# Optimization experiments

Hardware: AMD Instinct MI355X
Metric: run time of the kernel (lower is better)

Reference implementation:

```python
import jax, jax.numpy as jnp
import numpy as np

HIDDEN = 896
N_HEADS = 14
N_KV = 2
HEAD_DIM = HIDDEN // N_HEADS  # 64
N_REP = N_HEADS // N_KV       # 7
ROPE_THETA = 1000000.0


def setup_inputs() -> dict:
    key = jax.random.key(0)
    ks = jax.random.split(key, 8)
    B, S = 2, 2048
    s = 0.02
    return {
        "hidden_states": jax.random.normal(ks[0], (B, S, HIDDEN), dtype=jnp.float32),
        "position_ids": jnp.broadcast_to(jnp.arange(S, dtype=jnp.int64), (B, S)),
        "Wq": jax.random.normal(ks[1], (HIDDEN, HIDDEN), dtype=jnp.float32) * s,
        "bq": jnp.zeros((HIDDEN,), dtype=jnp.float32),
        "Wk": jax.random.normal(ks[2], (N_KV * HEAD_DIM, HIDDEN), dtype=jnp.float32) * s,
        "bk": jnp.zeros((N_KV * HEAD_DIM,), dtype=jnp.float32),
        "Wv": jax.random.normal(ks[3], (N_KV * HEAD_DIM, HIDDEN), dtype=jnp.float32) * s,
        "bv": jnp.zeros((N_KV * HEAD_DIM,), dtype=jnp.float32),
        "Wo": jax.random.normal(ks[4], (HIDDEN, HIDDEN), dtype=jnp.float32) * s,
    }


def _rotate_half(x):
    x1, x2 = x[..., : HEAD_DIM // 2], x[..., HEAD_DIM // 2 :]
    return jnp.concatenate((-x2, x1), axis=-1)


def reference(hidden_states, position_ids, Wq, bq, Wk, bk, Wv, bv, Wo):
    B, S, _ = hidden_states.shape
    q = (hidden_states @ Wq.T + bq).reshape(B, S, N_HEADS, HEAD_DIM)
    k = (hidden_states @ Wk.T + bk).reshape(B, S, N_KV, HEAD_DIM)
    v = (hidden_states @ Wv.T + bv).reshape(B, S, N_KV, HEAD_DIM)

    # RoPE: cos/sin [B, S, 1, HEAD_DIM]
    inv_freq = 1.0 / (ROPE_THETA ** (jnp.arange(0, HEAD_DIM, 2, dtype=jnp.float32) / HEAD_DIM))
    freqs = position_ids.astype(jnp.float32)[..., None] * inv_freq  # [B,S,D/2]
    emb = jnp.concatenate((freqs, freqs), axis=-1)
    cos = jnp.cos(emb)[:, :, None, :]
    sin = jnp.sin(emb)[:, :, None, :]
    q = q * cos + _rotate_half(q) * sin
    k = k * cos + _rotate_half(k) * sin

    # [B, H, S, D]; repeat KV heads (GQA)
    q = q.transpose(0, 2, 1, 3)
    k = jnp.repeat(k.transpose(0, 2, 1, 3), N_REP, axis=1)
    v = jnp.repeat(v.transpose(0, 2, 1, 3), N_REP, axis=1)

    scale = 1.0 / np.sqrt(HEAD_DIM)
    scores = jnp.einsum("bhqd,bhkd->bhqk", q, k) * scale
    causal = jnp.tril(jnp.ones((S, S), dtype=bool))
    scores = jnp.where(causal[None, None, :, :], scores, jnp.finfo(scores.dtype).min)
    probs = jax.nn.softmax(scores, axis=-1)
    attn = jnp.einsum("bhqk,bhkd->bhqd", probs, v)  # [B,H,S,D]
    attn = attn.transpose(0, 2, 1, 3).reshape(B, S, HIDDEN)
    return attn @ Wo.T
```

## Files before the change

kernel.cpp:

```cpp
#include <hip/hip_runtime.h>

#define HID 896
#define NH 14
#define NKV 2
#define NREP 7
#define SEQ 2048
#define BT 2
#define NTOK (BT*SEQ)
#define CSCALE 0.18033688011112042f

typedef __attribute__((ext_vector_type(8))) short bf16x8;
typedef __attribute__((ext_vector_type(8))) unsigned short u16x8;
typedef __attribute__((ext_vector_type(4))) float fx4;
typedef __attribute__((ext_vector_type(4))) short s16x4;
typedef _Float16 f16x4 __attribute__((ext_vector_type(4)));
typedef __fp16 fp16x2 __attribute__((ext_vector_type(2)));

#define LDA 136

__device__ __forceinline__ unsigned short f2b(float x){
  union { float f; unsigned u; } a; a.f = x;
  unsigned r = a.u + 0x7FFFu + ((a.u >> 16) & 1u);
  return (unsigned short)(r >> 16);
}
__device__ __forceinline__ unsigned short f2h(float x){
  union { _Float16 h; unsigned short u; } a; a.h = (_Float16)x; return a.u;
}

__global__ __launch_bounds__(256) void cvt_kernel(
    const float* __restrict__ s0, const float* __restrict__ s1,
    const float* __restrict__ s2, const float* __restrict__ s3,
    unsigned short* __restrict__ d0, unsigned short* __restrict__ d1,
    unsigned short* __restrict__ d2, unsigned short* __restrict__ d3,
    int c0, int c1, int c2, int c3,
    float2* __restrict__ tab)
{
  if (blockIdx.y == 4){
    for (int i = blockIdx.x*256 + threadIdx.x; i < SEQ*32; i += gridDim.x*256){
      int s = i >> 5, d = i & 31;
      float f = (float)s * exp2f(-(float)d * 0.62286151779138041f);
      float sv, cv; sincosf(f, &sv, &cv);
      tab[i] = make_float2(cv, sv);
    }
    return;
  }
  const float* s; unsigned short* d; int c;
  switch (blockIdx.y){
    case 0: s=s0; d=d0; c=c0; break;
    case 1: s=s1; d=d1; c=c1; break;
    case 2: s=s2; d=d2; c=c2; break;
    default: s=s3; d=d3; c=c3; break;
  }
  for (int i = (blockIdx.x*256 + threadIdx.x)*8; i < c; i += gridDim.x*2048){
    float4 a = *(const float4*)(s + i);
    float4 b = *(const float4*)(s + i + 4);
    u16x8 o;
    o[0]=f2b(a.x); o[1]=f2b(a.y); o[2]=f2b(a.z); o[3]=f2b(a.w);
    o[4]=f2b(b.x); o[5]=f2b(b.y); o[6]=f2b(b.z); o[7]=f2b(b.w);
    *(u16x8*)(d + i) = o;
  }
}

__global__ __launch_bounds__(256) void qkv_gemm_kernel(
    const float* __restrict__ hidden, const unsigned short* __restrict__ Bw,
    const float* __restrict__ bq, const float* __restrict__ bk, const float* __restrict__ bv,
    const int* __restrict__ pos, const float2* __restrict__ tab,
    unsigned short* __restrict__ qo, unsigned short* __restrict__ ko,
    unsigned short* __restrict__ vt)
{
  __shared__ short As[64*LDA];
  __shared__ short Bs[128*LDA];
  const int tid = threadIdx.x;
  const int bm = blockIdx.x, bn = blockIdx.y;
  const int w = tid >> 6, l = tid & 63, l15 = l & 15, q4 = l >> 4;
  const int wm = w >> 1, wn = w & 1;

  fx4 acc[2][4] = {};

  const int arow = tid >> 2, acol = (tid & 3)*32;
  const int brow = tid >> 1, bcol = (tid & 1)*64;
  const float* Agf = hidden + (size_t)(bm*64 + arow)*HID + acol;
  const unsigned short* Bg = Bw + (size_t)(bn*128 + brow)*HID + bcol;

  float4 a4[8]; u16x8 br[8];
#pragma unroll
  for (int p = 0; p < 8; p++) a4[p] = *(const float4*)(Agf + p*4);
#pragma unroll
  for (int p = 0; p < 8; p++) br[p] = *(const u16x8*)(Bg + p*8);

  for (int kt = 0; kt < 7; kt++){
#pragma unroll
    for (int p = 0; p < 4; p++){
      u16x8 av;
      av[0]=f2b(a4[2*p].x); av[1]=f2b(a4[2*p].y); av[2]=f2b(a4[2*p].z); av[3]=f2b(a4[2*p].w);
      av[4]=f2b(a4[2*p+1].x); av[5]=f2b(a4[2*p+1].y); av[6]=f2b(a4[2*p+1].z); av[7]=f2b(a4[2*p+1].w);
      *(u16x8*)&As[arow*LDA + acol + p*8] = av;
    }
#pragma unroll
    for (int p = 0; p < 8; p++) *(u16x8*)&Bs[brow*LDA + bcol + p*8] = br[p];
    __syncthreads();
    if (kt < 6){
      const int ko_ = (kt+1)*128;
#pragma unroll
      for (int p = 0; p < 8; p++) a4[p] = *(const float4*)(Agf + ko_ + p*4);
#pragma unroll
      for (int p = 0; p < 8; p++) br[p] = *(const u16x8*)(Bg + ko_ + p*8);
    }
#pragma unroll
    for (int ks = 0; ks < 4; ks++){
      bf16x8 af[2], bf[4];
#pragma unroll
      for (int mt = 0; mt < 2; mt++)
        af[mt] = *(bf16x8*)&As[(wm*32 + mt*16 + l15)*LDA + ks*32 + q4*8];
#pragma unroll
      for (int nt = 0; nt < 4; nt++)
        bf[nt] = *(bf16x8*)&Bs[(wn*64 + nt*16 + l15)*LDA + ks*32 + q4*8];
#pragma unroll
      for (int mt = 0; mt < 2; mt++)
#pragma unroll
        for (int nt = 0; nt < 4; nt++)
          acc[mt][nt] = __builtin_amdgcn_mfma_f32_16x16x32_bf16(af[mt], bf[nt], acc[mt][nt], 0,0,0);
    }
    __syncthreads();
  }

  const int hu = bn*2 + wn;
  const float* bias; int kind, hloc;
  if (hu < NH)      { bias = bq + hu*64;      kind = 0; hloc = hu; }
  else if (hu < 16) { bias = bk + (hu-NH)*64; kind = 1; hloc = hu-NH; }
  else              { bias = bv + (hu-16)*64; kind = 2; hloc = hu-16; }
  float bl[4];
#pragma unroll
  for (int nt = 0; nt < 4; nt++) bl[nt] = bias[nt*16 + l15];

  if (kind == 2){
#pragma unroll
    for (int mt = 0; mt < 2; mt++)
#pragma unroll
      for (int j = 0; j < 4; j++){
        int grow = bm*64 + wm*32 + mt*16 + q4*4 + j;
        int b = grow >> 11, s = grow & (SEQ-1);
        int tile = s >> 6, key = s & 63;
        unsigned short* dst = vt + (size_t)(((b*NKV + hloc)*(SEQ/64) + tile)*4096);
#pragma unroll
        for (int nt = 0; nt < 4; nt++)
          dst[(nt*16 + l15)*64 + key] = f2h(acc[mt][nt][j] + bl[nt]);
      }
  } else {
    const float qs = (kind == 0) ? CSCALE : 1.0f;
#pragma unroll
    for (int mt = 0; mt < 2; mt++)
#pragma unroll
      for (int j = 0; j < 4; j++){
        int grow = bm*64 + wm*32 + mt*16 + q4*4 + j;
        int b = grow >> 11, s = grow & (SEQ-1);
        int p = pos[grow];
        const float2* rp = tab + p*32 + l15;
        float2 cs0 = rp[0], cs1 = rp[16];
        unsigned short* dst = (kind == 0)
            ? qo + ((size_t)(b*NH  + hloc)*SEQ + s)*64
            : ko + ((size_t)(b*NKV + hloc)*SEQ + s)*64;
        float x1 = acc[mt][0][j] + bl[0], x2 = acc[mt][2][j] + bl[2];
        float y1 = acc[mt][1][j] + bl[1], y2 = acc[mt][3][j] + bl[3];
        dst[l15]      = f2b((x1*cs0.x - x2*cs0.y)*qs);
        dst[16 + l15] = f2b((y1*cs1.x - y2*cs1.y)*qs);
        dst[32 + l15] = f2b((x2*cs0.x + x1*cs0.y)*qs);
        dst[48 + l15] = f2b((y2*cs1.x + y1*cs1.y)*qs);
      }
  }
}

__device__ __forceinline__ void smax_pv(
    const fx4* s, bool diag, int wl, int q4,
    float& m_run, float& l_run, fx4* o, const f16x4 vf[4][4])
{
  float tv[16];
#pragma unroll
  for (int tl = 0; tl < 4; tl++)
#pragma unroll
    for (int j = 0; j < 4; j++){
      float x = s[tl][j];
      if (diag && (tl*16 + q4*4 + j > wl)) x = -1e30f;
      tv[tl*4+j] = x;
    }
  float mx = tv[0];
#pragma unroll
  for (int i = 1; i < 16; i++) mx = fmaxf(mx, tv[i]);
  mx = fmaxf(mx, __shfl_xor(mx, 16));
  mx = fmaxf(mx, __shfl_xor(mx, 32));
  float mn = fmaxf(m_run, mx);
  float al = exp2f(m_run - mn);
  m_run = mn;
  float p[16], rs = 0.f;
#pragma unroll
  for (int i = 0; i < 16; i++){ p[i] = exp2f(tv[i] - mn); rs += p[i]; }
  rs += __shfl_xor(rs, 16);
  rs += __shfl_xor(rs, 32);
  l_run = l_run*al + rs;
#pragma unroll
  for (int nt = 0; nt < 4; nt++)
#pragma unroll
    for (int j = 0; j < 4; j++) o[nt][j] *= al;
  f16x4 pf[4];
#pragma unroll
  for (int tl = 0; tl < 4; tl++){
    union { f16x4 v; fp16x2 h[2]; } u;
    u.h[0] = __builtin_amdgcn_cvt_pkrtz(p[tl*4+0], p[tl*4+1]);
    u.h[1] = __builtin_amdgcn_cvt_pkrtz(p[tl*4+2], p[tl*4+3]);
    pf[tl] = u.v;
  }
#pragma unroll
  for (int nt = 0; nt < 4; nt++)
#pragma unroll
    for (int tl = 0; tl < 4; tl++)
      o[nt] = __builtin_amdgcn_mfma_f32_16x16x16f16(vf[nt][tl], pf[tl], o[nt], 0,0,0);
}

__global__ __launch_bounds__(512) void attn_kernel(
    const unsigned short* __restrict__ q, const unsigned short* __restrict__ k,
    const unsigned short* __restrict__ vt, unsigned short* __restrict__ ao)
{
  __shared__ short SB[4*64*72];
  short* KsB = SB;
  short* VtB = SB + 2*64*72;

  const int tid = threadIdx.x;
  const int w = tid >> 6, l = tid & 63, l15 = l & 15, q4 = l >> 4;
  const int g = w >> 2, wi = w & 3;
  const int tlo = blockIdx.x, thi = 31 - tlo;
  const int h = blockIdx.y, b = blockIdx.z, kvh = h / NREP;
  const int wl = wi*16 + l15;

  const unsigned short* qbase = q + ((size_t)(b*NH + h)*SEQ)*64;
  const unsigned short* qpA = qbase + (size_t)(thi*64 + wl)*64;
  const unsigned short* qpB = qbase + (size_t)(tlo*64 + wl)*64;
  bf16x8 qA0 = *(const bf16x8*)(qpA + q4*8), qA1 = *(const bf16x8*)(qpA + 32 + q4*8);
  bf16x8 qB0 = *(const bf16x8*)(qpB + q4*8), qB1 = *(const bf16x8*)(qpB + 32 + q4*8);

  fx4 oA[4] = {}, oB[4] = {};
  float mA = -1e30f, lA = 0.f, mB = -1e30f, lB = 0.f;

  const unsigned short* kbase = k  + ((size_t)(b*NKV + kvh)*SEQ)*64;
  const unsigned short* vbase = vt + (size_t)((b*NKV + kvh)*(SEQ/64))*4096;

  const int P = (thi + 2) >> 1;

  u16x8 kreg[2], vreg[2];
#pragma unroll
  for (int p = 0; p < 2; p++){
    int idx = p*512 + tid, tile = idx >> 9, off = idx & 511;
    kreg[p] = *(const u16x8*)(kbase + (size_t)tile*4096 + off*8);
    vreg[p] = *(const u16x8*)(vbase + (size_t)tile*4096 + off*8);
  }

  for (int si = 0; si < P; si++){
#pragma unroll
    for (int p = 0; p < 2; p++){
      int idx = p*512 + tid, tile = idx >> 9, off = idx & 511;
      int rr = off >> 3, g8 = off & 7;
      *(u16x8*)&KsB[tile*4608 + rr*72 + g8*8] = kreg[p];
      *(u16x8*)&VtB[tile*4608 + rr*72 + g8*8] = vreg[p];
    }
    __syncthreads();

    if (si + 1 < P){
      const int k0n = 2*(si+1);
#pragma unroll
      for (int p = 0; p < 2; p++){
        int idx = p*512 + tid, tile = idx >> 9, off = idx & 511;
        int tk = k0n + tile; if (tk > thi) tk = thi;
        kreg[p] = *(const u16x8*)(kbase + (size_t)tk*4096 + off*8);
        vreg[p] = *(const u16x8*)(vbase + (size_t)tk*4096 + off*8);
      }
    }

    const int kt = 2*si + g;
    if (kt <= thi){
      const short* Kst = KsB + g*4608;
      const short* Vtt = VtB + g*4608;
      bf16x8 kf0[4], kf1[4];
#pragma unroll
      for (int tl = 0; tl < 4; tl++){
        kf0[tl] = *(const bf16x8*)&Kst[(tl*16 + l15)*72 + q4*8];
        kf1[tl] = *(const bf16x8*)&Kst[(tl*16 + l15)*72 + 32 + q4*8];
      }
      f16x4 vf[4][4];
#pragma unroll
      for (int nt = 0; nt < 4; nt++)
#pragma unroll
        for (int tl = 0; tl < 4; tl++)
          vf[nt][tl] = *(const f16x4*)&Vtt[(nt*16 + l15)*72 + tl*16 + q4*4];

      {
        fx4 s[4] = {};
#pragma unroll
        for (int tl = 0; tl < 4; tl++){
          s[tl] = __builtin_amdgcn_mfma_f32_16x16x32_bf16(kf0[tl], qA0, s[tl], 0,0,0);
          s[tl] = __builtin_amdgcn_mfma_f32_16x16x32_bf16(kf1[tl], qA1, s[tl], 0,0,0);
        }
        smax_pv(s, kt == thi, wl, q4, mA, lA, oA, vf);
      }
      if (kt <= tlo){
        fx4 s[4] = {};
#pragma unroll
        for (int tl = 0; tl < 4; tl++){
          s[tl] = __builtin_amdgcn_mfma_f32_16x16x32_bf16(kf0[tl], qB0, s[tl], 0,0,0);
          s[tl] = __builtin_amdgcn_mfma_f32_16x16x32_bf16(kf1[tl], qB1, s[tl], 0,0,0);
        }
        smax_pv(s, kt == tlo, wl, q4, mB, lB, oB, vf);
      }
    }
    __syncthreads();
  }

  float* F = (float*)SB;
  if (g == 1){
    float* fa = F + (((wi*2 + 0)*64 + l)*18);
#pragma unroll
    for (int nt = 0; nt < 4; nt++)
#pragma unroll
      for (int j = 0; j < 4; j++) fa[nt*4 + j] = oA[nt][j];
    fa[16] = mA; fa[17] = lA;
    float* fb = F + (((wi*2 + 1)*64 + l)*18);
#pragma unroll
    for (int nt = 0; nt < 4; nt++)
#pragma unroll
      for (int j = 0; j < 4; j++) fb[nt*4 + j] = oB[nt][j];
    fb[16] = mB; fb[17] = lB;
  }
  __syncthreads();
  if (g == 0){
    {
      const float* fa = F + (((wi*2 + 0)*64 + l)*18);
      float m1 = fa[16], l1 = fa[17];
      float mM = fmaxf(mA, m1);
      float a0 = exp2f(mA - mM), a1 = exp2f(m1 - mM);
      lA = lA*a0 + l1*a1;
#pragma unroll
      for (int nt = 0; nt < 4; nt++)
#pragma unroll
        for (int j = 0; j < 4; j++) oA[nt][j] = oA[nt][j]*a0 + fa[nt*4+j]*a1;
    }
    {
      const float* fb = F + (((wi*2 + 1)*64 + l)*18);
      float m1 = fb[16], l1 = fb[17];
      float mM = fmaxf(mB, m1);
      float a0 = exp2f(mB - mM), a1 = exp2f(m1 - mM);
      lB = lB*a0 + l1*a1;
#pragma unroll
      for (int nt = 0; nt < 4; nt++)
#pragma unroll
        for (int j = 0; j < 4; j++) oB[nt][j] = oB[nt][j]*a0 + fb[nt*4+j]*a1;
    }
    {
      float inv = 1.0f / lA;
      unsigned short* dst = ao + ((size_t)(b*SEQ + thi*64 + wl))*HID + h*64;
#pragma unroll
      for (int nt = 0; nt < 4; nt++){
        s16x4 ov;
        ov[0] = (short)f2b(oA[nt][0]*inv); ov[1] = (short)f2b(oA[nt][1]*inv);
        ov[2] = (short)f2b(oA[nt][2]*inv); ov[3] = (short)f2b(oA[nt][3]*inv);
        *(s16x4*)(dst + nt*16 + q4*4) = ov;
      }
    }
    {
      float inv = 1.0f / lB;
      unsigned short* dst = ao + ((size_t)(b*SEQ + tlo*64 + wl))*HID + h*64;
#pragma unroll
      for (int nt = 0; nt < 4; nt++){
        s16x4 ov;
        ov[0] = (short)f2b(oB[nt][0]*inv); ov[1] = (short)f2b(oB[nt][1]*inv);
        ov[2] = (short)f2b(oB[nt][2]*inv); ov[3] = (short)f2b(oB[nt][3]*inv);
        *(s16x4*)(dst + nt*16 + q4*4) = ov;
      }
    }
  }
}

__global__ __launch_bounds__(256) void out_gemm_kernel(
    const unsigned short* __restrict__ A, const unsigned short* __restrict__ Bw,
    float* __restrict__ out)
{
  __shared__ short As[64*LDA];
  __shared__ short Bs[128*LDA];
  const int tid = threadIdx.x;
  const int bm = blockIdx.x, bn = blockIdx.y;
  const int w = tid >> 6, l = tid & 63, l15 = l & 15, q4 = l >> 4;
  const int wm = w >> 1, wn = w & 1;

  fx4 acc[2][4] = {};

  const int arow = tid >> 2, acol = (tid & 3)*32;
  const int brow = tid >> 1, bcol = (tid & 1)*64;
  const unsigned short* Ag = A  + (size_t)(bm*64  + arow)*HID + acol;
  const unsigned short* Bg = Bw + (size_t)(bn*128 + brow)*HID + bcol;

  u16x8 ar[4], br[8];
#pragma unroll
  for (int p = 0; p < 4; p++) ar[p] = *(const u16x8*)(Ag + p*8);
#pragma unroll
  for (int p = 0; p < 8; p++) br[p] = *(const u16x8*)(Bg + p*8);

  for (int kt = 0; kt < 7; kt++){
#pragma unroll
    for (int p = 0; p < 4; p++) *(u16x8*)&As[arow*LDA + acol + p*8] = ar[p];
#pragma unroll
    for (int p = 0; p < 8; p++) *(u16x8*)&Bs[brow*LDA + bcol + p*8] = br[p];
    __syncthreads();
    if (kt < 6){
      const int ko_ = (kt+1)*128;
#pragma unroll
      for (int p = 0; p < 4; p++) ar[p] = *(const u16x8*)(Ag + ko_ + p*8);
#pragma unroll
      for (int p = 0; p < 8; p++) br[p] = *(const u16x8*)(Bg + ko_ + p*8);
    }
#pragma unroll
    for (int ks = 0; ks < 4; ks++){
      bf16x8 af[2], bf[4];
#pragma unroll
      for (int mt = 0; mt < 2; mt++)
        af[mt] = *(bf16x8*)&As[(wm*32 + mt*16 + l15)*LDA + ks*32 + q4*8];
#pragma unroll
      for (int nt = 0; nt < 4; nt++)
        bf[nt] = *(bf16x8*)&Bs[(wn*64 + nt*16 + l15)*LDA + ks*32 + q4*8];
#pragma unroll
      for (int mt = 0; mt < 2; mt++)
#pragma unroll
        for (int nt = 0; nt < 4; nt++)
          acc[mt][nt] = __builtin_amdgcn_mfma_f32_16x16x32_bf16(af[mt], bf[nt], acc[mt][nt], 0,0,0);
    }
    __syncthreads();
  }

#pragma unroll
  for (int mt = 0; mt < 2; mt++)
#pragma unroll
    for (int j = 0; j < 4; j++){
      int grow = bm*64 + wm*32 + mt*16 + q4*4 + j;
      float* dst = out + (size_t)grow*HID + bn*128 + wn*64;
#pragma unroll
      for (int nt = 0; nt < 4; nt++)
        dst[nt*16 + l15] = acc[mt][nt][j];
    }
}

extern "C" void kernel_launch(void* const* d_in, const int* in_sizes, int n_in,
                              void* d_out, int out_size, void* d_ws, size_t ws_size,
                              hipStream_t stream)
{
  const float* hidden = (const float*)d_in[0];
  const int*   pos    = (const int*)d_in[1];
  const float* Wq = (const float*)d_in[2]; const float* bq = (const float*)d_in[3];
  const float* Wk = (const float*)d_in[4]; const float* bk = (const float*)d_in[5];
  const float* Wv = (const float*)d_in[6]; const float* bv = (const float*)d_in[7];
  const float* Wo = (const float*)d_in[8];

  unsigned short* qws   = (unsigned short*)d_ws;
  unsigned short* kws   = qws   + (size_t)BT*NH*SEQ*64;
  unsigned short* vtws  = kws   + (size_t)BT*NKV*SEQ*64;
  unsigned short* wqkv  = vtws  + (size_t)BT*NKV*SEQ*64;
  unsigned short* wo16  = wqkv  + (size_t)1152*HID;
  unsigned short* h16   = wo16  + (size_t)HID*HID;
  float2*         tab   = (float2*)(h16 + (size_t)NTOK*HID);

  const int nwq  = HID*HID;
  const int nwkv = 2*64*HID;

  cvt_kernel<<<dim3(392, 5), 256, 0, stream>>>(
      Wq, Wk, Wv, Wo,
      wqkv, wqkv + nwq, wqkv + nwq + nwkv, wo16,
      nwq, nwkv, nwkv, nwq, tab);

  qkv_gemm_kernel<<<dim3(NTOK/64, 9), 256, 0, stream>>>(
      hidden, wqkv, bq, bk, bv, pos, tab, qws, kws, vtws);

  attn_kernel<<<dim3(16, NH, BT), 512, 0, stream>>>(qws, kws, vtws, h16);

  out_gemm_kernel<<<dim3(NTOK/64, 7), 256, 0, stream>>>(h16, wo16, (float*)d_out);
}
```

Measured before the change: 201.4 us.

## Use direct global-to-LDS loads with XOR swizzle in projection GEMMs

Both projection GEMMs now stage tiles through global_load_lds (direct global-to-LDS DMA) into an unpadded 64-wide LDS tile with XOR swizzling, instead of loading into registers and storing to padded shared memory. The K tile shrinks from 128 to 64, giving 14 iterations. The hidden-state fp32-to-bf16 conversion moves into the pre-pass cvt kernel so the QKV GEMM reads bf16. The aim is to cut register staging and VGPR pressure, but the register-prefetch overlap is lost: each iteration now loads and then syncs with no double buffering, and the hidden states take an extra round trip through memory. h16 is reused as the attention output buffer, which is safe only because the QKV GEMM finishes before attention writes it.

```diff
diff --git a/kernel.cpp b/kernel.cpp
--- a/kernel.cpp
+++ b/kernel.cpp
@@ -16,8 +16,6 @@
 typedef _Float16 f16x4 __attribute__((ext_vector_type(4)));
 typedef __fp16 fp16x2 __attribute__((ext_vector_type(2)));
 
-#define LDA 136
-
 __device__ __forceinline__ unsigned short f2b(float x){
   union { float f; unsigned u; } a; a.f = x;
   unsigned r = a.u + 0x7FFFu + ((a.u >> 16) & 1u);
@@ -27,15 +25,23 @@
   union { _Float16 h; unsigned short u; } a; a.h = (_Float16)x; return a.u;
 }
 
+__device__ __forceinline__ void gll16(const unsigned short* g, short* lds){
+  __builtin_amdgcn_global_load_lds(
+      (const __attribute__((address_space(1))) unsigned int*)(const void*)g,
+      (__attribute__((address_space(3))) unsigned int*)(void*)lds, 16, 0, 0);
+}
+
 __global__ __launch_bounds__(256) void cvt_kernel(
     const float* __restrict__ s0, const float* __restrict__ s1,
     const float* __restrict__ s2, const float* __restrict__ s3,
+    const float* __restrict__ s4,
     unsigned short* __restrict__ d0, unsigned short* __restrict__ d1,
     unsigned short* __restrict__ d2, unsigned short* __restrict__ d3,
-    int c0, int c1, int c2, int c3,
+    unsigned short* __restrict__ d4,
+    int c0, int c1, int c2, int c3, int c4,
     float2* __restrict__ tab)
 {
-  if (blockIdx.y == 4){
+  if (blockIdx.y == 5){
     for (int i = blockIdx.x*256 + threadIdx.x; i < SEQ*32; i += gridDim.x*256){
       int s = i >> 5, d = i & 31;
       float f = (float)s * exp2f(-(float)d * 0.62286151779138041f);
@@ -49,7 +55,8 @@
     case 0: s=s0; d=d0; c=c0; break;
     case 1: s=s1; d=d1; c=c1; break;
     case 2: s=s2; d=d2; c=c2; break;
-    default: s=s3; d=d3; c=c3; break;
+    case 3: s=s3; d=d3; c=c3; break;
+    default: s=s4; d=d4; c=c4; break;
   }
   for (int i = (blockIdx.x*256 + threadIdx.x)*8; i < c; i += gridDim.x*2048){
     float4 a = *(const float4*)(s + i);
@@ -62,59 +69,53 @@
 }
 
 __global__ __launch_bounds__(256) void qkv_gemm_kernel(
-    const float* __restrict__ hidden, const unsigned short* __restrict__ Bw,
+    const unsigned short* __restrict__ A, const unsigned short* __restrict__ Bw,
     const float* __restrict__ bq, const float* __restrict__ bk, const float* __restrict__ bv,
     const int* __restrict__ pos, const float2* __restrict__ tab,
     unsigned short* __restrict__ qo, unsigned short* __restrict__ ko,
     unsigned short* __restrict__ vt)
 {
-  __shared__ short As[64*LDA];
-  __shared__ short Bs[128*LDA];
+  __shared__ short As[64*64];
+  __shared__ short Bs[128*64];
   const int tid = threadIdx.x;
   const int bm = blockIdx.x, bn = blockIdx.y;
   const int w = tid >> 6, l = tid & 63, l15 = l & 15, q4 = l >> 4;
   const int wm = w >> 1, wn = w & 1;
+  const int lr = l >> 3;
+  const int cbg = (l & 7) ^ lr;
+  const int sw = l15 & 7;
 
   fx4 acc[2][4] = {};
 
-  const int arow = tid >> 2, acol = (tid & 3)*32;
-  const int brow = tid >> 1, bcol = (tid & 1)*64;
-  const float* Agf = hidden + (size_t)(bm*64 + arow)*HID + acol;
-  const unsigned short* Bg = Bw + (size_t)(bn*128 + brow)*HID + bcol;
-
-  float4 a4[8]; u16x8 br[8];
-#pragma unroll
-  for (int p = 0; p < 8; p++) a4[p] = *(const float4*)(Agf + p*4);
-#pragma unroll
-  for (int p = 0; p < 8; p++) br[p] = *(const u16x8*)(Bg + p*8);
-
-  for (int kt = 0; kt < 7; kt++){
+  const unsigned short* Ag = A  + (size_t)(bm*64)*HID;
+  const unsigned short* Bg = Bw + (size_t)(bn*128)*HID;
+
+  for (int kt = 0; kt < 14; kt++){
+    const int kc = kt*64 + cbg*8;
+#pragma unroll
+    for (int p = 0; p < 2; p++){
+      int c = p*4 + w;
+      gll16(Ag + (size_t)(c*8 + lr)*HID + kc, &As[c*512]);
+    }
 #pragma unroll
     for (int p = 0; p < 4; p++){
-      u16x8 av;
-      av[0]=f2b(a4[2*p].x); av[1]=f2b(a4[2*p].y); av[2]=f2b(a4[2*p].z); av[3]=f2b(a4[2*p].w);
-      av[4]=f2b(a4[2*p+1].x); av[5]=f2b(a4[2*p+1].y); av[6]=f2b(a4[2*p+1].z); av[7]=f2b(a4[2*p+1].w);
-      *(u16x8*)&As[arow*LDA + acol + p*8] = av;
-    }
-#pragma unroll
-    for (int p = 0; p < 8; p++) *(u16x8*)&Bs[brow*LDA + bcol + p*8] = br[p];
-    __syncthreads();
-    if (kt < 6){
-      const int ko_ = (kt+1)*128;
-#pragma unroll
-      for (int p = 0; p < 8; p++) a4[p] = *(const float4*)(Agf + ko_ + p*4);
-#pragma unroll
-      for (int p = 0; p < 8; p++) br[p] = *(const u16x8*)(Bg + ko_ + p*8);
-    }
-#pragma unroll
-    for (int ks = 0; ks < 4; ks++){
+      int c = p*4 + w;
+      gll16(Bg + (size_t)(c*8 + lr)*HID + kc, &Bs[c*512]);
+    }
+    __syncthreads();
+#pragma unroll
+    for (int ks = 0; ks < 2; ks++){
       bf16x8 af[2], bf[4];
 #pragma unroll
-      for (int mt = 0; mt < 2; mt++)
-        af[mt] = *(bf16x8*)&As[(wm*32 + mt*16 + l15)*LDA + ks*32 + q4*8];
-#pragma unroll
-      for (int nt = 0; nt < 4; nt++)
-        bf[nt] = *(bf16x8*)&Bs[(wn*64 + nt*16 + l15)*LDA + ks*32 + q4*8];
+      for (int mt = 0; mt < 2; mt++){
+        int r = wm*32 + mt*16 + l15;
+        af[mt] = *(bf16x8*)&As[r*64 + ((ks*4 + q4) ^ sw)*8];
+      }
+#pragma unroll
+      for (int nt = 0; nt < 4; nt++){
+        int r = wn*64 + nt*16 + l15;
+        bf[nt] = *(bf16x8*)&Bs[r*64 + ((ks*4 + q4) ^ sw)*8];
+      }
 #pragma unroll
       for (int mt = 0; mt < 2; mt++)
 #pragma unroll
@@ -381,48 +382,47 @@
     const unsigned short* __restrict__ A, const unsigned short* __restrict__ Bw,
     float* __restrict__ out)
 {
-  __shared__ short As[64*LDA];
-  __shared__ short Bs[128*LDA];
+  __shared__ short As[64*64];
+  __shared__ short Bs[128*64];
   const int tid = threadIdx.x;
   const int bm = blockIdx.x, bn = blockIdx.y;
   const int w = tid >> 6, l = tid & 63, l15 = l & 15, q4 = l >> 4;
   const int wm = w >> 1, wn = w & 1;
+  const int lr = l >> 3;
+  const int cbg = (l & 7) ^ lr;
+  const int sw = l15 & 7;
 
   fx4 acc[2][4] = {};
 
-  const int arow = tid >> 2, acol = (tid & 3)*32;
-  const int brow = tid >> 1, bcol = (tid & 1)*64;
-  const unsigned short* Ag = A  + (size_t)(bm*64  + arow)*HID + acol;
-  const unsigned short* Bg = Bw + (size_t)(bn*128 + brow)*HID + bcol;
-
-  u16x8 ar[4], br[8];
-#pragma unroll
-  for (int p = 0; p < 4; p++) ar[p] = *(const u16x8*)(Ag + p*8);
-#pragma unroll
-  for (int p = 0; p < 8; p++) br[p] = *(const u16x8*)(Bg + p*8);
-
-  for (int kt = 0; kt < 7; kt++){
-#pragma unroll
-    for (int p = 0; p < 4; p++) *(u16x8*)&As[arow*LDA + acol + p*8] = ar[p];
-#pragma unroll
-    for (int p = 0; p < 8; p++) *(u16x8*)&Bs[brow*LDA + bcol + p*8] = br[p];
-    __syncthreads();
-    if (kt < 6){
-      const int ko_ = (kt+1)*128;
-#pragma unroll
-      for (int p = 0; p < 4; p++) ar[p] = *(const u16x8*)(Ag + ko_ + p*8);
-#pragma unroll
-      for (int p = 0; p < 8; p++) br[p] = *(const u16x8*)(Bg + ko_ + p*8);
-    }
-#pragma unroll
-    for (int ks = 0; ks < 4; ks++){
+  const unsigned short* Ag = A  + (size_t)(bm*64)*HID;
+  const unsigned short* Bg = Bw + (size_t)(bn*128)*HID;
+
+  for (int kt = 0; kt < 14; kt++){
+    const int kc = kt*64 + cbg*8;
+#pragma unroll
+    for (int p = 0; p < 2; p++){
+      int c = p*4 + w;
+      gll16(Ag + (size_t)(c*8 + lr)*HID + kc, &As[c*512]);
+    }
+#pragma unroll
+    for (int p = 0; p < 4; p++){
+      int c = p*4 + w;
+      gll16(Bg + (size_t)(c*8 + lr)*HID + kc, &Bs[c*512]);
+    }
+    __syncthreads();
+#pragma unroll
+    for (int ks = 0; ks < 2; ks++){
       bf16x8 af[2], bf[4];
 #pragma unroll
-      for (int mt = 0; mt < 2; mt++)
-        af[mt] = *(bf16x8*)&As[(wm*32 + mt*16 + l15)*LDA + ks*32 + q4*8];
-#pragma unroll
-      for (int nt = 0; nt < 4; nt++)
-        bf[nt] = *(bf16x8*)&Bs[(wn*64 + nt*16 + l15)*LDA + ks*32 + q4*8];
+      for (int mt = 0; mt < 2; mt++){
+        int r = wm*32 + mt*16 + l15;
+        af[mt] = *(bf16x8*)&As[r*64 + ((ks*4 + q4) ^ sw)*8];
+      }
+#pragma unroll
+      for (int nt = 0; nt < 4; nt++){
+        int r = wn*64 + nt*16 + l15;
+        bf[nt] = *(bf16x8*)&Bs[r*64 + ((ks*4 + q4) ^ sw)*8];
+      }
 #pragma unroll
       for (int mt = 0; mt < 2; mt++)
 #pragma unroll
@@ -463,16 +463,17 @@
   unsigned short* h16   = wo16  + (size_t)HID*HID;
   float2*         tab   = (float2*)(h16 + (size_t)NTOK*HID);
 
+  const int nh   = NTOK*HID;
   const int nwq  = HID*HID;
   const int nwkv = 2*64*HID;
 
-  cvt_kernel<<<dim3(392, 5), 256, 0, stream>>>(
-      Wq, Wk, Wv, Wo,
-      wqkv, wqkv + nwq, wqkv + nwq + nwkv, wo16,
-      nwq, nwkv, nwkv, nwq, tab);
+  cvt_kernel<<<dim3(448, 6), 256, 0, stream>>>(
+      hidden, Wq, Wk, Wv, Wo,
+      h16, wqkv, wqkv + nwq, wqkv + nwq + nwkv, wo16,
+      nh, nwq, nwkv, nwkv, nwq, tab);
 
   qkv_gemm_kernel<<<dim3(NTOK/64, 9), 256, 0, stream>>>(
-      hidden, wqkv, bq, bk, bv, pos, tab, qws, kws, vtws);
+      h16, wqkv, bq, bk, bv, pos, tab, qws, kws, vtws);
 
   attn_kernel<<<dim3(16, NH, BT), 512, 0, stream>>>(qws, kws, vtws, h16);
 
```

New measurement: 164.6 us (median of 2 runs). 18.3% less time.
